# Kernel optimization log

Measured on AMD Instinct MI355X. Metric: run time of the kernel, lower is better.

## Reference

```python
import jax, jax.numpy as jnp
import numpy as np

C_IN = 512
C = 64        # per-head dim
N_HEAD = 8
B, S = 2, 2048


def setup_inputs() -> dict:
    key = jax.random.key(0)
    ks = jax.random.split(key, 9)
    scale = 1.0 / np.sqrt(C_IN)
    return {
        "x": jax.random.normal(ks[0], (B, S, C_IN), dtype=jnp.float32),
        "bias": jax.random.normal(ks[1], (B, N_HEAD, S, S), dtype=jnp.float32),
        "Wq": jax.random.normal(ks[2], (N_HEAD * C, C_IN), dtype=jnp.float32) * scale,
        "Wk": jax.random.normal(ks[3], (N_HEAD * C, C_IN), dtype=jnp.float32) * scale,
        "Wv": jax.random.normal(ks[4], (N_HEAD * C, C_IN), dtype=jnp.float32) * scale,
        "Wo": jax.random.normal(ks[5], (C_IN, N_HEAD * C), dtype=jnp.float32) * scale,
        "bo": jax.random.normal(ks[6], (C_IN,), dtype=jnp.float32) * 0.01,
        "Wg": jax.random.normal(ks[7], (N_HEAD * C, C_IN), dtype=jnp.float32) * scale,
        "bg": jax.random.normal(ks[8], (N_HEAD * C,), dtype=jnp.float32) * 0.01,
    }


def reference(x, bias, Wq, Wk, Wv, Wo, bo, Wg, bg):
    # x: [B, S, C_IN]; attn_dim=1 -> q/k/v axis is already at -2 after movedim.
    # Project and split heads: [B, S, H*C] -> [B, H, S, C]
    def split_heads(t):
        Bq, Sq, _ = t.shape
        return t.reshape(Bq, Sq, N_HEAD, C).transpose(0, 2, 1, 3)

    q = split_heads(x @ Wq.T) / jnp.sqrt(jnp.asarray(C, x.dtype))
    k = split_heads(x @ Wk.T)
    v = split_heads(x @ Wv.T)

    a = jnp.einsum("bhqc,bhkc->bhqk", q, k) + bias   # [B, H, S, S]
    a = jax.nn.softmax(a, axis=-1)
    o = jnp.einsum("bhqk,bhkc->bhqc", a, v)          # [B, H, S, C]

    # merge heads back: [B, S, H*C]
    o = o.transpose(0, 2, 1, 3).reshape(x.shape[0], x.shape[1], N_HEAD * C)
    g = jax.nn.sigmoid(x @ Wg.T + bg)
    o = g * o
    return o @ Wo.T + bo                              # [B, S, C_IN]
```

## Files before the change

kernel.cpp:

```cpp
#include <hip/hip_runtime.h>
#include <math.h>

#define BB 2
#define HH 8
#define SS 2048
#define CC 64
#define CIN 512
#define DDIM 512
#define MM (BB*SS)
#define KSPLIT 2
#define KDOM (SS / KSPLIT)
#define NCHUNK (KDOM / 64)

#define SOFTMAX_SHIFT 16.0f

using short8  = __attribute__((ext_vector_type(8))) short;
using float4v = __attribute__((ext_vector_type(4))) float;

__device__ __forceinline__ unsigned short tob(float f) {
    unsigned u = __float_as_uint(f);
    unsigned r = (u + 0x7fffu + ((u >> 16) & 1u)) >> 16;
    return (unsigned short)r;
}
__device__ __forceinline__ float fromb(unsigned short u) {
    return __uint_as_float(((unsigned)u) << 16);
}

__global__ __launch_bounds__(256) void convert_all(
    const float* __restrict__ x,
    const float* __restrict__ wq, const float* __restrict__ wk,
    const float* __restrict__ wv, const float* __restrict__ wg,
    const float* __restrict__ wo,
    unsigned short* __restrict__ xb,
    unsigned short* __restrict__ wqb, unsigned short* __restrict__ wkb,
    unsigned short* __restrict__ wvb, unsigned short* __restrict__ wgb,
    unsigned short* __restrict__ wob)
{
    const int NX4 = MM * CIN / 4;
    int i = blockIdx.x * blockDim.x + threadIdx.x;
    const float* src; unsigned short* dst; float scale = 1.0f; int off;
    if (i < NX4) { src = x; dst = xb; off = i; }
    else {
        int j = i - NX4;
        int seg = j >> 16;
        off = j & 65535;
        if      (seg == 0) { src = wq; dst = wqb; scale = 0.125f; }
        else if (seg == 1) { src = wk; dst = wkb; }
        else if (seg == 2) { src = wv; dst = wvb; }
        else if (seg == 3) { src = wg; dst = wgb; }
        else               { src = wo; dst = wob; }
    }
    float4 v = ((const float4*)src)[off];
    ushort4 o;
    o.x = tob(v.x * scale); o.y = tob(v.y * scale);
    o.z = tob(v.z * scale); o.w = tob(v.w * scale);
    ((ushort4*)dst)[off] = o;
}

__global__ __launch_bounds__(256) void proj_gemm(
    const unsigned short* __restrict__ X,
    const unsigned short* __restrict__ Wq,
    const unsigned short* __restrict__ Wk,
    const unsigned short* __restrict__ Wv,
    const unsigned short* __restrict__ Wg,
    const float* __restrict__ bg,
    unsigned short* __restrict__ Qd,
    unsigned short* __restrict__ Kd,
    unsigned short* __restrict__ Vd,
    unsigned short* __restrict__ Gd)
{
    __shared__ __align__(16) unsigned short At[64][72];
    __shared__ __align__(16) unsigned short Bt[64][72];

    int mode = blockIdx.z;
    const unsigned short* W = (mode == 0) ? Wq : (mode == 1) ? Wk : (mode == 2) ? Wv : Wg;

    int m0 = blockIdx.y * 64;
    int n0 = blockIdx.x * 64;
    int tid = threadIdx.x;
    int w = tid >> 6, lane = tid & 63;
    int quad = lane >> 4, l16 = lane & 15;
    int wm = w & 1, wn = w >> 1;

    float4v acc[2][2];
    for (int a = 0; a < 2; ++a) for (int c = 0; c < 2; ++c) acc[a][c] = (float4v)0.0f;

    for (int kc = 0; kc < CIN; kc += 64) {
        for (int it = 0; it < 2; ++it) {
            int idx = it * 2048 + tid * 8;
            int row = idx >> 6, col = idx & 63;
            *(short8*)&At[row][col] = *(const short8*)&X[(size_t)(m0 + row) * CIN + kc + col];
            *(short8*)&Bt[row][col] = *(const short8*)&W[(size_t)(n0 + row) * CIN + kc + col];
        }
        __syncthreads();
        for (int ks = 0; ks < 2; ++ks) {
            short8 a0 = *(const short8*)&At[wm * 32 + l16][ks * 32 + quad * 8];
            short8 a1 = *(const short8*)&At[wm * 32 + 16 + l16][ks * 32 + quad * 8];
            short8 b0 = *(const short8*)&Bt[wn * 32 + l16][ks * 32 + quad * 8];
            short8 b1 = *(const short8*)&Bt[wn * 32 + 16 + l16][ks * 32 + quad * 8];
            acc[0][0] = __builtin_amdgcn_mfma_f32_16x16x32_bf16(a0, b0, acc[0][0], 0, 0, 0);
            acc[0][1] = __builtin_amdgcn_mfma_f32_16x16x32_bf16(a0, b1, acc[0][1], 0, 0, 0);
            acc[1][0] = __builtin_amdgcn_mfma_f32_16x16x32_bf16(a1, b0, acc[1][0], 0, 0, 0);
            acc[1][1] = __builtin_amdgcn_mfma_f32_16x16x32_bf16(a1, b1, acc[1][1], 0, 0, 0);
        }
        __syncthreads();
    }

    if (mode == 2) {
        for (int a = 0; a < 2; ++a) for (int c = 0; c < 2; ++c)
            for (int r = 0; r < 4; ++r) {
                int ml = wm * 32 + a * 16 + quad * 4 + r;
                int nl = wn * 32 + c * 16 + l16;
                At[nl][ml] = tob(acc[a][c][r]);
            }
        __syncthreads();
        int bi = m0 >> 11, h = n0 >> 6, s0 = m0 & 2047;
        int crow = tid >> 2, seg = tid & 3;
        unsigned short* dp = Vd + (((size_t)(bi * HH + h) * CC) + crow) * SS + s0 + seg * 16;
        *(short8*)dp       = *(const short8*)&At[crow][seg * 16];
        *(short8*)(dp + 8) = *(const short8*)&At[crow][seg * 16 + 8];
        return;
    }

    for (int a = 0; a < 2; ++a) for (int c = 0; c < 2; ++c)
        for (int r = 0; r < 4; ++r) {
            int gm = m0 + wm * 32 + a * 16 + quad * 4 + r;
            int gn = n0 + wn * 32 + c * 16 + l16;
            float v = acc[a][c][r];
            if (mode <= 1) {
                int bi = gm >> 11, s = gm & 2047, h = gn >> 6, cc = gn & 63;
                unsigned short* d = (mode == 0) ? Qd : Kd;
                d[(((size_t)(bi * HH + h) * SS) + s) * CC + cc] = tob(v);
            } else {
                float g = 1.0f / (1.0f + __expf(-(v + bg[gn])));
                Gd[(size_t)gm * DDIM + gn] = tob(g);
            }
        }
}

__global__ __launch_bounds__(256) void attn_kernel(
    const unsigned short* __restrict__ Q,
    const unsigned short* __restrict__ K,
    const unsigned short* __restrict__ V,
    const float* __restrict__ bias,
    float* __restrict__ part,
    float* __restrict__ Ls)
{
    __shared__ __align__(16) unsigned short Kt[64][72];
    __shared__ __align__(16) unsigned short Vt[64][72];
    __shared__ __align__(16) unsigned short Pt[4][16][72];

    int qb = blockIdx.x * 64;
    int bh = blockIdx.y;
    int split = blockIdx.z;
    int ksbase = split * KDOM;
    int b = bh >> 3, h = bh & 7;
    int tid = threadIdx.x;
    int w = tid >> 6, lane = tid & 63;
    int quad = lane >> 4, l16 = lane & 15;

    const unsigned short* Qbh = Q + (size_t)bh * SS * CC;
    const unsigned short* Kbh = K + (size_t)bh * SS * CC + (size_t)ksbase * CC;
    const unsigned short* Vbh = V + (size_t)bh * CC * SS + ksbase;
    const float* biasbh = bias + (size_t)bh * SS * SS + ksbase;

    int qrow = qb + w * 16 + l16;
    short8 aq0 = *(const short8*)&Qbh[(size_t)qrow * CC + quad * 8];
    short8 aq1 = *(const short8*)&Qbh[(size_t)qrow * CC + 32 + quad * 8];

    float lsum[4] = {0.f, 0.f, 0.f, 0.f};
    float4v accO[4];
    for (int jn = 0; jn < 4; ++jn) accO[jn] = (float4v)0.0f;

    int srow0 = (tid * 8) >> 6,        scol0 = (tid * 8) & 63;
    int srow1 = (2048 + tid * 8) >> 6, scol1 = (2048 + tid * 8) & 63;

    const float* brow[4];
    for (int r = 0; r < 4; ++r)
        brow[r] = biasbh + (size_t)(qb + w * 16 + quad * 4 + r) * SS + l16;

    short8 pk0[2], pv0[2], pk1[2], pv1[2];
    float  bb0[4][4], bb1[4][4];
    pk0[0] = *(const short8*)&Kbh[(size_t)srow0 * CC + scol0];
    pk0[1] = *(const short8*)&Kbh[(size_t)srow1 * CC + scol1];
    pv0[0] = *(const short8*)&Vbh[(size_t)srow0 * SS + scol0];
    pv0[1] = *(const short8*)&Vbh[(size_t)srow1 * SS + scol1];
    for (int j = 0; j < 4; ++j)
        for (int r = 0; r < 4; ++r)
            bb0[j][r] = brow[r][j * 16];

#pragma unroll
    for (int c = 0; c < NCHUNK; ++c) {
        int kb  = c * 64;
        int kbn = (c + 1 < NCHUNK ? c + 1 : c) * 64;
        const bool even = (c & 1) == 0;
        short8* pkc = even ? pk0 : pk1;
        short8* pvc = even ? pv0 : pv1;
        short8* pkn = even ? pk1 : pk0;
        short8* pvn = even ? pv1 : pv0;
        float (*bbc)[4] = even ? bb0 : bb1;
        float (*bbn)[4] = even ? bb1 : bb0;

        __syncthreads();
        *(short8*)&Kt[srow0][scol0] = pkc[0];
        *(short8*)&Kt[srow1][scol1] = pkc[1];
        *(short8*)&Vt[srow0][scol0] = pvc[0];
        *(short8*)&Vt[srow1][scol1] = pvc[1];

        pkn[0] = *(const short8*)&Kbh[(size_t)(kbn + srow0) * CC + scol0];
        pkn[1] = *(const short8*)&Kbh[(size_t)(kbn + srow1) * CC + scol1];
        pvn[0] = *(const short8*)&Vbh[(size_t)srow0 * SS + kbn + scol0];
        pvn[1] = *(const short8*)&Vbh[(size_t)srow1 * SS + kbn + scol1];
        for (int j = 0; j < 4; ++j)
            for (int r = 0; r < 4; ++r)
                bbn[j][r] = brow[r][kbn + j * 16];

        __syncthreads();

        float4v sa[4];
        for (int j = 0; j < 4; ++j) sa[j] = (float4v)0.0f;
        for (int j = 0; j < 4; ++j) {
            short8 bk0 = *(const short8*)&Kt[j * 16 + l16][quad * 8];
            short8 bk1 = *(const short8*)&Kt[j * 16 + l16][32 + quad * 8];
            sa[j] = __builtin_amdgcn_mfma_f32_16x16x32_bf16(aq0, bk0, sa[j], 0, 0, 0);
            sa[j] = __builtin_amdgcn_mfma_f32_16x16x32_bf16(aq1, bk1, sa[j], 0, 0, 0);
        }

        for (int j = 0; j < 4; ++j)
            for (int r = 0; r < 4; ++r) {
                float p = __expf(sa[j][r] + bbc[j][r] - SOFTMAX_SHIFT);
                lsum[r] += p;
                Pt[w][quad * 4 + r][j * 16 + l16] = tob(p);
            }

        for (int ks = 0; ks < 2; ++ks) {
            short8 ap = *(const short8*)&Pt[w][l16][ks * 32 + quad * 8];
            for (int jn = 0; jn < 4; ++jn) {
                short8 bv = *(const short8*)&Vt[jn * 16 + l16][ks * 32 + quad * 8];
                accO[jn] = __builtin_amdgcn_mfma_f32_16x16x32_bf16(ap, bv, accO[jn], 0, 0, 0);
            }
        }
    }

    for (int r = 0; r < 4; ++r) {
        float s = lsum[r];
        s += __shfl_xor(s, 1, 64);
        s += __shfl_xor(s, 2, 64);
        s += __shfl_xor(s, 4, 64);
        s += __shfl_xor(s, 8, 64);
        lsum[r] = s;
    }

    int mrow = b * SS + qb + w * 16 + quad * 4;
    float* pOut = part + (size_t)split * MM * DDIM;
    for (int jn = 0; jn < 4; ++jn)
        for (int r = 0; r < 4; ++r)
            pOut[(size_t)(mrow + r) * DDIM + h * 64 + jn * 16 + l16] = accO[jn][r];
    if (l16 == 0)
        for (int r = 0; r < 4; ++r)
            Ls[((size_t)split * MM + mrow + r) * HH + h] = lsum[r];
}

__global__ __launch_bounds__(256) void combine_kernel(
    const float* __restrict__ part,
    const float* __restrict__ Ls,
    const unsigned short* __restrict__ G,
    unsigned short* __restrict__ Og)
{
    int i = blockIdx.x * 256 + threadIdx.x;
    int row = i >> 7;
    int c4  = (i & 127) << 2;
    int h   = c4 >> 6;
    float l = Ls[(size_t)row * HH + h] + Ls[((size_t)MM + row) * HH + h];
    float rl = 1.0f / l;
    const float4* p0 = (const float4*)(part) + ((size_t)row * DDIM + c4) / 4;
    const float4* p1 = (const float4*)(part + (size_t)MM * DDIM) + ((size_t)row * DDIM + c4) / 4;
    float4 a = *p0, bq = *p1;
    ushort4 g = *(const ushort4*)&G[(size_t)row * DDIM + c4];
    ushort4 o;
    o.x = tob((a.x + bq.x) * rl * fromb(g.x));
    o.y = tob((a.y + bq.y) * rl * fromb(g.y));
    o.z = tob((a.z + bq.z) * rl * fromb(g.z));
    o.w = tob((a.w + bq.w) * rl * fromb(g.w));
    *(ushort4*)&Og[(size_t)row * DDIM + c4] = o;
}

__global__ __launch_bounds__(256) void out_gemm(
    const unsigned short* __restrict__ Og,
    const unsigned short* __restrict__ W,
    const float* __restrict__ bo,
    float* __restrict__ out)
{
    __shared__ __align__(16) unsigned short At[64][72];
    __shared__ __align__(16) unsigned short Bt[64][72];

    int m0 = blockIdx.y * 64;
    int n0 = blockIdx.x * 64;
    int tid = threadIdx.x;
    int w = tid >> 6, lane = tid & 63;
    int quad = lane >> 4, l16 = lane & 15;
    int wm = w & 1, wn = w >> 1;

    float4v acc[2][2];
    for (int a = 0; a < 2; ++a) for (int c = 0; c < 2; ++c) acc[a][c] = (float4v)0.0f;

    for (int kc = 0; kc < DDIM; kc += 64) {
        for (int it = 0; it < 2; ++it) {
            int idx = it * 2048 + tid * 8;
            int row = idx >> 6, col = idx & 63;
            *(short8*)&At[row][col] = *(const short8*)&Og[(size_t)(m0 + row) * DDIM + kc + col];
            *(short8*)&Bt[row][col] = *(const short8*)&W[(size_t)(n0 + row) * DDIM + kc + col];
        }
        __syncthreads();
        for (int ks = 0; ks < 2; ++ks) {
            short8 a0 = *(const short8*)&At[wm * 32 + l16][ks * 32 + quad * 8];
            short8 a1 = *(const short8*)&At[wm * 32 + 16 + l16][ks * 32 + quad * 8];
            short8 b0 = *(const short8*)&Bt[wn * 32 + l16][ks * 32 + quad * 8];
            short8 b1 = *(const short8*)&Bt[wn * 32 + 16 + l16][ks * 32 + quad * 8];
            acc[0][0] = __builtin_amdgcn_mfma_f32_16x16x32_bf16(a0, b0, acc[0][0], 0, 0, 0);
            acc[0][1] = __builtin_amdgcn_mfma_f32_16x16x32_bf16(a0, b1, acc[0][1], 0, 0, 0);
            acc[1][0] = __builtin_amdgcn_mfma_f32_16x16x32_bf16(a1, b0, acc[1][0], 0, 0, 0);
            acc[1][1] = __builtin_amdgcn_mfma_f32_16x16x32_bf16(a1, b1, acc[1][1], 0, 0, 0);
        }
        __syncthreads();
    }

    for (int a = 0; a < 2; ++a) for (int c = 0; c < 2; ++c)
        for (int r = 0; r < 4; ++r) {
            int gm = m0 + wm * 32 + a * 16 + quad * 4 + r;
            int gn = n0 + wn * 32 + c * 16 + l16;
            out[(size_t)gm * DDIM + gn] = acc[a][c][r] + bo[gn];
        }
}

extern "C" void kernel_launch(void* const* d_in, const int* in_sizes, int n_in,
                              void* d_out, int out_size, void* d_ws, size_t ws_size,
                              hipStream_t stream)
{
    const float* x    = (const float*)d_in[0];
    const float* bias = (const float*)d_in[1];
    const float* Wq   = (const float*)d_in[2];
    const float* Wk   = (const float*)d_in[3];
    const float* Wv   = (const float*)d_in[4];
    const float* Wo   = (const float*)d_in[5];
    const float* bo   = (const float*)d_in[6];
    const float* Wg   = (const float*)d_in[7];
    const float* bg   = (const float*)d_in[8];
    float* out = (float*)d_out;

    char* ws = (char*)d_ws;
    auto alloc = [&](size_t bytes) { char* p = ws; ws += (bytes + 255) & ~(size_t)255; return p; };
    unsigned short* xb  = (unsigned short*)alloc((size_t)MM * CIN * 2);
    unsigned short* wqb = (unsigned short*)alloc((size_t)DDIM * CIN * 2);
    unsigned short* wkb = (unsigned short*)alloc((size_t)DDIM * CIN * 2);
    unsigned short* wvb = (unsigned short*)alloc((size_t)DDIM * CIN * 2);
    unsigned short* wgb = (unsigned short*)alloc((size_t)DDIM * CIN * 2);
    unsigned short* wob = (unsigned short*)alloc((size_t)DDIM * CIN * 2);
    unsigned short* Qh  = (unsigned short*)alloc((size_t)BB * HH * SS * CC * 2);
    unsigned short* Kh  = (unsigned short*)alloc((size_t)BB * HH * SS * CC * 2);
    unsigned short* Vh  = (unsigned short*)alloc((size_t)BB * HH * SS * CC * 2);
    unsigned short* Gt  = (unsigned short*)alloc((size_t)MM * DDIM * 2);
    unsigned short* Om  = (unsigned short*)alloc((size_t)MM * DDIM * 2);
    float* part = (float*)alloc((size_t)KSPLIT * MM * DDIM * 4);
    float* Lsum = (float*)alloc((size_t)KSPLIT * MM * HH * 4);

    convert_all<<<3328, 256, 0, stream>>>(x, Wq, Wk, Wv, Wg, Wo,
                                          xb, wqb, wkb, wvb, wgb, wob);
    proj_gemm<<<dim3(DDIM / 64, MM / 64, 4), 256, 0, stream>>>(
        xb, wqb, wkb, wvb, wgb, bg, Qh, Kh, Vh, Gt);
    attn_kernel<<<dim3(SS / 64, BB * HH, KSPLIT), 256, 0, stream>>>(
        Qh, Kh, Vh, bias, part, Lsum);
    combine_kernel<<<(MM * DDIM / 4) / 256, 256, 0, stream>>>(part, Lsum, Gt, Om);
    out_gemm<<<dim3(DDIM / 64, MM / 64), 256, 0, stream>>>(Om, wob, bo, out);
}
```

Measured before the change: 435.8 us.

## Use 128x128 tiles in fused QKVG projection and store attention partials as bf16

The projection GEMM now uses 128x128 tiles over a single concatenated weight matrix, indexing it through wqb on the assumption that wqb, wkb, wvb and wgb sit contiguously in the workspace. Each warp computes a 64x64 sub-tile with 16 MFMA accumulators, giving more operand reuse per LDS load and fewer blocks. Separately, the split-K attention partial outputs are stored as bf16 instead of fp32, halving their write and read traffic in the combine step. This costs some precision in the partial sums, and the contiguity assumption depends on the alloc padding (256-byte rounding of exact 512 KB buffers, which holds here).

```diff
diff --git a/kernel.cpp b/kernel.cpp
--- a/kernel.cpp
+++ b/kernel.cpp
@@ -8,6 +8,7 @@
 #define CIN 512
 #define DDIM 512
 #define MM (BB*SS)
+#define NTOT 2048
 #define KSPLIT 2
 #define KDOM (SS / KSPLIT)
 #define NCHUNK (KDOM / 64)
@@ -57,85 +58,95 @@
     ((ushort4*)dst)[off] = o;
 }
 
-__global__ __launch_bounds__(256) void proj_gemm(
+__global__ __launch_bounds__(256) void proj_gemm128(
     const unsigned short* __restrict__ X,
-    const unsigned short* __restrict__ Wq,
-    const unsigned short* __restrict__ Wk,
-    const unsigned short* __restrict__ Wv,
-    const unsigned short* __restrict__ Wg,
+    const unsigned short* __restrict__ Wcat,
     const float* __restrict__ bg,
     unsigned short* __restrict__ Qd,
     unsigned short* __restrict__ Kd,
     unsigned short* __restrict__ Vd,
     unsigned short* __restrict__ Gd)
 {
-    __shared__ __align__(16) unsigned short At[64][72];
-    __shared__ __align__(16) unsigned short Bt[64][72];
-
-    int mode = blockIdx.z;
-    const unsigned short* W = (mode == 0) ? Wq : (mode == 1) ? Wk : (mode == 2) ? Wv : Wg;
-
-    int m0 = blockIdx.y * 64;
-    int n0 = blockIdx.x * 64;
+    __shared__ __align__(16) unsigned short At[128][72];
+    __shared__ __align__(16) unsigned short Bt[128][72];
+
+    int n0 = blockIdx.x * 128;
+    int m0 = blockIdx.y * 128;
+    int mode = n0 >> 9;
     int tid = threadIdx.x;
     int w = tid >> 6, lane = tid & 63;
     int quad = lane >> 4, l16 = lane & 15;
     int wm = w & 1, wn = w >> 1;
 
-    float4v acc[2][2];
-    for (int a = 0; a < 2; ++a) for (int c = 0; c < 2; ++c) acc[a][c] = (float4v)0.0f;
+    float4v acc[4][4];
+    for (int i = 0; i < 4; ++i) for (int j = 0; j < 4; ++j) acc[i][j] = (float4v)0.0f;
+
+    int srow = tid >> 3, scol = (tid & 7) * 8;
 
     for (int kc = 0; kc < CIN; kc += 64) {
-        for (int it = 0; it < 2; ++it) {
-            int idx = it * 2048 + tid * 8;
-            int row = idx >> 6, col = idx & 63;
-            *(short8*)&At[row][col] = *(const short8*)&X[(size_t)(m0 + row) * CIN + kc + col];
-            *(short8*)&Bt[row][col] = *(const short8*)&W[(size_t)(n0 + row) * CIN + kc + col];
+        for (int it = 0; it < 4; ++it) {
+            int row = it * 32 + srow;
+            *(short8*)&At[row][scol] = *(const short8*)&X[(size_t)(m0 + row) * CIN + kc + scol];
+            *(short8*)&Bt[row][scol] = *(const short8*)&Wcat[(size_t)(n0 + row) * CIN + kc + scol];
         }
         __syncthreads();
         for (int ks = 0; ks < 2; ++ks) {
-            short8 a0 = *(const short8*)&At[wm * 32 + l16][ks * 32 + quad * 8];
-            short8 a1 = *(const short8*)&At[wm * 32 + 16 + l16][ks * 32 + quad * 8];
-            short8 b0 = *(const short8*)&Bt[wn * 32 + l16][ks * 32 + quad * 8];
-            short8 b1 = *(const short8*)&Bt[wn * 32 + 16 + l16][ks * 32 + quad * 8];
-            acc[0][0] = __builtin_amdgcn_mfma_f32_16x16x32_bf16(a0, b0, acc[0][0], 0, 0, 0);
-            acc[0][1] = __builtin_amdgcn_mfma_f32_16x16x32_bf16(a0, b1, acc[0][1], 0, 0, 0);
-            acc[1][0] = __builtin_amdgcn_mfma_f32_16x16x32_bf16(a1, b0, acc[1][0], 0, 0, 0);
-            acc[1][1] = __builtin_amdgcn_mfma_f32_16x16x32_bf16(a1, b1, acc[1][1], 0, 0, 0);
-        }
-        __syncthreads();
-    }
+            short8 a[4], b[4];
+            for (int i = 0; i < 4; ++i)
+                a[i] = *(const short8*)&At[wm * 64 + i * 16 + l16][ks * 32 + quad * 8];
+            for (int j = 0; j < 4; ++j)
+                b[j] = *(const short8*)&Bt[wn * 64 + j * 16 + l16][ks * 32 + quad * 8];
+            for (int i = 0; i < 4; ++i)
+                for (int j = 0; j < 4; ++j)
+                    acc[i][j] = __builtin_amdgcn_mfma_f32_16x16x32_bf16(a[i], b[j], acc[i][j], 0, 0, 0);
+        }
+        __syncthreads();
+    }
+
+    int bi = m0 >> 11, s0 = m0 & 2047;
 
     if (mode == 2) {
-        for (int a = 0; a < 2; ++a) for (int c = 0; c < 2; ++c)
+        unsigned short* scratch = (unsigned short*)At;
+        for (int hh = 0; hh < 2; ++hh) {
+            if (wn == hh) {
+                for (int i = 0; i < 4; ++i)
+                    for (int j = 0; j < 4; ++j)
+                        for (int r = 0; r < 4; ++r) {
+                            int c = j * 16 + l16;
+                            int s = wm * 64 + i * 16 + quad * 4 + r;
+                            scratch[c * 136 + s] = tob(acc[i][j][r]);
+                        }
+            }
+            __syncthreads();
+            int h = ((n0 & 511) >> 6) + hh;
+            int c = tid >> 2, q4 = tid & 3;
+            unsigned short* dp = Vd + (((size_t)(bi * HH + h) * CC) + c) * SS + s0 + q4 * 32;
+            const unsigned short* sp = scratch + c * 136 + q4 * 32;
+            *(short8*)(dp)      = *(const short8*)(sp);
+            *(short8*)(dp + 8)  = *(const short8*)(sp + 8);
+            *(short8*)(dp + 16) = *(const short8*)(sp + 16);
+            *(short8*)(dp + 24) = *(const short8*)(sp + 24);
+            __syncthreads();
+        }
+        return;
+    }
+
+    for (int i = 0; i < 4; ++i)
+        for (int j = 0; j < 4; ++j)
             for (int r = 0; r < 4; ++r) {
-                int ml = wm * 32 + a * 16 + quad * 4 + r;
-                int nl = wn * 32 + c * 16 + l16;
-                At[nl][ml] = tob(acc[a][c][r]);
+                int gm = m0 + wm * 64 + i * 16 + quad * 4 + r;
+                int gnl = (n0 & 511) + wn * 64 + j * 16 + l16;
+                float v = acc[i][j][r];
+                int s = gm & 2047;
+                if (mode <= 1) {
+                    int h = gnl >> 6, c = gnl & 63;
+                    unsigned short* d = (mode == 0) ? Qd : Kd;
+                    d[(((size_t)(bi * HH + h) * SS) + s) * CC + c] = tob(v);
+                } else {
+                    float g = 1.0f / (1.0f + __expf(-(v + bg[gnl])));
+                    Gd[(size_t)gm * DDIM + gnl] = tob(g);
+                }
             }
-        __syncthreads();
-        int bi = m0 >> 11, h = n0 >> 6, s0 = m0 & 2047;
-        int crow = tid >> 2, seg = tid & 3;
-        unsigned short* dp = Vd + (((size_t)(bi * HH + h) * CC) + crow) * SS + s0 + seg * 16;
-        *(short8*)dp       = *(const short8*)&At[crow][seg * 16];
-        *(short8*)(dp + 8) = *(const short8*)&At[crow][seg * 16 + 8];
-        return;
-    }
-
-    for (int a = 0; a < 2; ++a) for (int c = 0; c < 2; ++c)
-        for (int r = 0; r < 4; ++r) {
-            int gm = m0 + wm * 32 + a * 16 + quad * 4 + r;
-            int gn = n0 + wn * 32 + c * 16 + l16;
-            float v = acc[a][c][r];
-            if (mode <= 1) {
-                int bi = gm >> 11, s = gm & 2047, h = gn >> 6, cc = gn & 63;
-                unsigned short* d = (mode == 0) ? Qd : Kd;
-                d[(((size_t)(bi * HH + h) * SS) + s) * CC + cc] = tob(v);
-            } else {
-                float g = 1.0f / (1.0f + __expf(-(v + bg[gn])));
-                Gd[(size_t)gm * DDIM + gn] = tob(g);
-            }
-        }
 }
 
 __global__ __launch_bounds__(256) void attn_kernel(
@@ -143,7 +154,7 @@
     const unsigned short* __restrict__ K,
     const unsigned short* __restrict__ V,
     const float* __restrict__ bias,
-    float* __restrict__ part,
+    unsigned short* __restrict__ part,
     float* __restrict__ Ls)
 {
     __shared__ __align__(16) unsigned short Kt[64][72];
@@ -191,7 +202,6 @@
 
 #pragma unroll
     for (int c = 0; c < NCHUNK; ++c) {
-        int kb  = c * 64;
         int kbn = (c + 1 < NCHUNK ? c + 1 : c) * 64;
         const bool even = (c & 1) == 0;
         short8* pkc = even ? pk0 : pk1;
@@ -252,17 +262,17 @@
     }
 
     int mrow = b * SS + qb + w * 16 + quad * 4;
-    float* pOut = part + (size_t)split * MM * DDIM;
+    unsigned short* pOut = part + (size_t)split * MM * DDIM;
     for (int jn = 0; jn < 4; ++jn)
         for (int r = 0; r < 4; ++r)
-            pOut[(size_t)(mrow + r) * DDIM + h * 64 + jn * 16 + l16] = accO[jn][r];
+            pOut[(size_t)(mrow + r) * DDIM + h * 64 + jn * 16 + l16] = tob(accO[jn][r]);
     if (l16 == 0)
         for (int r = 0; r < 4; ++r)
             Ls[((size_t)split * MM + mrow + r) * HH + h] = lsum[r];
 }
 
 __global__ __launch_bounds__(256) void combine_kernel(
-    const float* __restrict__ part,
+    const unsigned short* __restrict__ part,
     const float* __restrict__ Ls,
     const unsigned short* __restrict__ G,
     unsigned short* __restrict__ Og)
@@ -273,16 +283,16 @@
     int h   = c4 >> 6;
     float l = Ls[(size_t)row * HH + h] + Ls[((size_t)MM + row) * HH + h];
     float rl = 1.0f / l;
-    const float4* p0 = (const float4*)(part) + ((size_t)row * DDIM + c4) / 4;
-    const float4* p1 = (const float4*)(part + (size_t)MM * DDIM) + ((size_t)row * DDIM + c4) / 4;
-    float4 a = *p0, bq = *p1;
-    ushort4 g = *(const ushort4*)&G[(size_t)row * DDIM + c4];
+    size_t off = (size_t)row * DDIM + c4;
+    ushort4 a0 = *(const ushort4*)&part[off];
+    ushort4 a1 = *(const ushort4*)&part[(size_t)MM * DDIM + off];
+    ushort4 g  = *(const ushort4*)&G[off];
     ushort4 o;
-    o.x = tob((a.x + bq.x) * rl * fromb(g.x));
-    o.y = tob((a.y + bq.y) * rl * fromb(g.y));
-    o.z = tob((a.z + bq.z) * rl * fromb(g.z));
-    o.w = tob((a.w + bq.w) * rl * fromb(g.w));
-    *(ushort4*)&Og[(size_t)row * DDIM + c4] = o;
+    o.x = tob((fromb(a0.x) + fromb(a1.x)) * rl * fromb(g.x));
+    o.y = tob((fromb(a0.y) + fromb(a1.y)) * rl * fromb(g.y));
+    o.z = tob((fromb(a0.z) + fromb(a1.z)) * rl * fromb(g.z));
+    o.w = tob((fromb(a0.w) + fromb(a1.w)) * rl * fromb(g.w));
+    *(ushort4*)&Og[off] = o;
 }
 
 __global__ __launch_bounds__(256) void out_gemm(
@@ -361,13 +371,13 @@
     unsigned short* Vh  = (unsigned short*)alloc((size_t)BB * HH * SS * CC * 2);
     unsigned short* Gt  = (unsigned short*)alloc((size_t)MM * DDIM * 2);
     unsigned short* Om  = (unsigned short*)alloc((size_t)MM * DDIM * 2);
-    float* part = (float*)alloc((size_t)KSPLIT * MM * DDIM * 4);
+    unsigned short* part = (unsigned short*)alloc((size_t)KSPLIT * MM * DDIM * 2);
     float* Lsum = (float*)alloc((size_t)KSPLIT * MM * HH * 4);
 
     convert_all<<<3328, 256, 0, stream>>>(x, Wq, Wk, Wv, Wg, Wo,
                                           xb, wqb, wkb, wvb, wgb, wob);
-    proj_gemm<<<dim3(DDIM / 64, MM / 64, 4), 256, 0, stream>>>(
-        xb, wqb, wkb, wvb, wgb, bg, Qh, Kh, Vh, Gt);
+    proj_gemm128<<<dim3(NTOT / 128, MM / 128), 256, 0, stream>>>(
+        xb, wqb, bg, Qh, Kh, Vh, Gt);
     attn_kernel<<<dim3(SS / 64, BB * HH, KSPLIT), 256, 0, stream>>>(
         Qh, Kh, Vh, bias, part, Lsum);
     combine_kernel<<<(MM * DDIM / 4) / 256, 256, 0, stream>>>(part, Lsum, Gt, Om);
```

Result: slower. 535.4 us (+22.9%).
